# Performance work log

Hardware: AMD Instinct MI355X
Metric: run time of the kernel (lower is better)

The kernel has to match this reference:

```python
import jax, jax.numpy as jnp
import numpy as np

ATTN_HEADS = 4
NEG_INF = float(np.finfo(np.float32).min)


def setup_inputs() -> dict:
    key = jax.random.key(0)
    ks = jax.random.split(key, 7)
    B, N, K, Cin, Cout = 4, 4096, 32, 128, 128
    h_X = jax.random.normal(ks[0], (B, N, Cout), dtype=jnp.float32)
    h_E = jax.random.normal(ks[1], (B, N, K, Cin), dtype=jnp.float32)
    mask_attn = jax.random.randint(ks[2], (B, N, K), 0, 2, dtype=jnp.int32)
    # torch Linear weights are [out_features, in_features]
    W_Q = jax.random.normal(ks[3], (Cout, Cout), dtype=jnp.float32) / np.sqrt(Cout)
    W_K = jax.random.normal(ks[4], (Cout, Cin), dtype=jnp.float32) / np.sqrt(Cin)
    W_V = jax.random.normal(ks[5], (Cout, Cin), dtype=jnp.float32) / np.sqrt(Cin)
    W_O = jax.random.normal(ks[6], (Cout, 3 * Cout), dtype=jnp.float32) / np.sqrt(3 * Cout)
    return {"h_X": h_X, "h_E": h_E, "mask_attn": mask_attn,
            "W_Q": W_Q, "W_K": W_K, "W_V": W_V, "W_O": W_O}


def reference(h_X, h_E, mask_attn, W_Q, W_K, W_V, W_O):
    B, N, K, _ = h_E.shape
    C = W_Q.shape[0]
    H = ATTN_HEADS
    d = C // H

    h_q = (h_X @ W_Q.T).reshape(B, N, H, d)          # [B,N,H,d]
    h_k = (h_E @ W_K.T).reshape(B, N, K, H, d)       # [B,N,K,H,d]
    h_v = (h_E @ W_V.T).reshape(B, N, K, H, d)       # [B,N,K,H,d]

    # per-node, per-head scores over K neighbors
    scores = jnp.einsum('bnhd,bnkhd->bnhk', h_q, h_k) / np.sqrt(d)

    mask = (mask_attn[:, :, None, :] > 0)            # [B,N,1,K] -> broadcast over heads
    logits = jnp.where(mask, scores, NEG_INF)
    attn = jax.nn.softmax(logits, axis=-1) * mask.astype(scores.dtype)  # [B,N,H,K]

    attn_sum = attn.sum(axis=-1, keepdims=True) + 1e-8                  # [B,N,H,1]
    hv_t = jnp.swapaxes(h_v, 2, 3)                                      # [B,N,H,K,d]
    weighted_v = attn[..., None] * hv_t                                 # [B,N,H,K,d]
    weighted_sum = weighted_v.sum(axis=3)                               # [B,N,H,d]
    aggr_mean = (weighted_sum / attn_sum).reshape(B, N, C)
    aggr_sum = weighted_sum.reshape(B, N, C)
    aggr_max = weighted_v.max(axis=3).reshape(B, N, C)

    aggr_cat = jnp.concatenate([aggr_mean, aggr_sum, aggr_max], axis=-1)  # [B,N,3C]
    return aggr_cat @ W_O.T                                               # [B,N,C]
```

## Files before the change

kernel.cpp:

```cpp
#include <hip/hip_runtime.h>
#include <stdint.h>


typedef __attribute__((ext_vector_type(8))) short short8;
typedef __attribute__((ext_vector_type(4))) float f32x4;

#define NPB   16
#define CDIM  128
#define KN    32
#define ESTR  136
#define TSTR  136
#define QSTR  136
#define CATS  392
#define SSTR  36

__device__ __forceinline__ float bf2f(short s) {
    union { unsigned int u; float f; } v;
    v.u = ((unsigned int)(unsigned short)s) << 16;
    return v.f;
}
__device__ __forceinline__ short f2bf(float f) {
    union { float ff; unsigned int u; } v; v.ff = f;
    unsigned int u = v.u;
    u += 0x7FFFu + ((u >> 16) & 1u);
    return (short)(u >> 16);
}

template<bool FP32>
__device__ __forceinline__ short8 load8bf(const void* p, size_t idx) {
    if constexpr (FP32) {
        const float* fp = (const float*)p + idx;
        f32x4 a = *(const f32x4*)fp;
        f32x4 b = *(const f32x4*)(fp + 4);
        short8 r;
        r[0] = f2bf(a[0]); r[1] = f2bf(a[1]); r[2] = f2bf(a[2]); r[3] = f2bf(a[3]);
        r[4] = f2bf(b[0]); r[5] = f2bf(b[1]); r[6] = f2bf(b[2]); r[7] = f2bf(b[3]);
        return r;
    } else {
        return *(const short8*)((const short*)p + idx);
    }
}

template<bool FP32>
__device__ __forceinline__ short loadbf1(const void* p, size_t idx) {
    if constexpr (FP32) return f2bf(((const float*)p)[idx]);
    else return ((const short*)p)[idx];
}

struct alignas(16) Smem {
    short sE[128 * ESTR];
    short sT[64 * TSTR];
    short sQ[16 * QSTR];
    short sCat[16 * CATS];
    float sS[16 * SSTR];
    int   sMask[NPB * KN];
};

template<bool FP32>
__device__ __forceinline__ void issueE(const void* hE, size_t base, int tid,
                                       f32x4 (&eF)[8][2], short8 (&eB)[8]) {
    if constexpr (FP32) {
        #pragma unroll
        for (int it = 0; it < 8; ++it) {
            const float* p = (const float*)hE + base + (size_t)(it * 256 + tid) * 8;
            eF[it][0] = *(const f32x4*)p;
            eF[it][1] = *(const f32x4*)(p + 4);
        }
    } else {
        #pragma unroll
        for (int it = 0; it < 8; ++it)
            eB[it] = *(const short8*)((const short*)hE + base + (size_t)(it * 256 + tid) * 8);
    }
    __builtin_amdgcn_sched_barrier(0);
}

template<bool FP32>
__device__ __forceinline__ void writeE(short* sE, int tid,
                                       const f32x4 (&eF)[8][2], const short8 (&eB)[8]) {
    #pragma unroll
    for (int it = 0; it < 8; ++it) {
        const int chunk = it * 256 + tid, row = chunk >> 4, cc = chunk & 15;
        short8 v;
        if constexpr (FP32) {
            #pragma unroll
            for (int t = 0; t < 4; ++t) { v[t] = f2bf(eF[it][0][t]); v[4 + t] = f2bf(eF[it][1][t]); }
        } else v = eB[it];
        *(short8*)&sE[row * ESTR + cc * 8] = v;
    }
}

template<bool FP32>
__device__ __forceinline__ void na_body(Smem& sm,
    const void* __restrict__ hX, const void* __restrict__ hE,
    const int* __restrict__ mask, const void* __restrict__ WQ,
    const void* __restrict__ WK, const void* __restrict__ WV,
    const void* __restrict__ WO, void* __restrict__ out)
{
    const int tid  = threadIdx.x;
    const int lane = tid & 63;
    const int w    = tid >> 6;
    const int quad = lane >> 4;
    const int l15  = lane & 15;
    const int nb   = blockIdx.x * NPB;
    const size_t ebase = (size_t)nb * (KN * CDIM);

    f32x4 eF[8][2]; short8 eB[8];
    issueE<FP32>(hE, ebase, tid, eF, eB);

    *(int2*)&sm.sMask[tid * 2] = *(const int2*)&mask[(size_t)nb * KN + tid * 2];

    short8 ax[4];
    #pragma unroll
    for (int kk = 0; kk < 4; ++kk)
        ax[kk] = load8bf<FP32>(hX, (size_t)(nb + l15) * CDIM + kk * 32 + quad * 8);

    short8 bq[2][4];
    #pragma unroll
    for (int t2 = 0; t2 < 2; ++t2)
        #pragma unroll
        for (int kk = 0; kk < 4; ++kk)
            bq[t2][kk] = load8bf<FP32>(WQ, (size_t)(w * 32 + t2 * 16 + l15) * CDIM + kk * 32 + quad * 8);

    short8 bk[2][4];
    #pragma unroll
    for (int t2 = 0; t2 < 2; ++t2)
        #pragma unroll
        for (int kk = 0; kk < 4; ++kk) {
            const int j = w * 32 + t2 * 16 + l15;
            short8 b;
            #pragma unroll
            for (int jj = 0; jj < 8; ++jj)
                b[jj] = loadbf1<FP32>(WK, (size_t)(kk * 32 + quad * 8 + jj) * CDIM + j);
            bk[t2][kk] = b;
        }

    {
        f32x4 o0 = {0.f,0.f,0.f,0.f}, o1 = {0.f,0.f,0.f,0.f};
        #pragma unroll
        for (int kk = 0; kk < 4; ++kk) {
            o0 = __builtin_amdgcn_mfma_f32_16x16x32_bf16(ax[kk], bq[0][kk], o0, 0, 0, 0);
            o1 = __builtin_amdgcn_mfma_f32_16x16x32_bf16(ax[kk], bq[1][kk], o1, 0, 0, 0);
        }
        #pragma unroll
        for (int r = 0; r < 4; ++r) {
            const int n = quad * 4 + r;
            sm.sQ[n * QSTR + w * 32 + l15]      = f2bf(o0[r]);
            sm.sQ[n * QSTR + w * 32 + 16 + l15] = f2bf(o1[r]);
        }
    }
    __syncthreads();

    {
        const float scale = 0.17677669529663687f;
        const short8 zz = {0,0,0,0,0,0,0,0};
        #pragma unroll
        for (int m = 0; m < 4; ++m) {
            const int n_g = m * 4 + (l15 >> 2), h_ = l15 & 3;
            const short8 qv = *(const short8*)&sm.sQ[n_g * QSTR + h_ * 32 + quad * 8];
            f32x4 c0 = {0.f,0.f,0.f,0.f}, c1 = {0.f,0.f,0.f,0.f};
            #pragma unroll
            for (int kk = 0; kk < 4; ++kk) {
                const short8 af = (kk == h_) ? qv : zz;
                c0 = __builtin_amdgcn_mfma_f32_16x16x32_bf16(af, bk[0][kk], c0, 0, 0, 0);
                c1 = __builtin_amdgcn_mfma_f32_16x16x32_bf16(af, bk[1][kk], c1, 0, 0, 0);
            }
            #pragma unroll
            for (int r = 0; r < 4; ++r) {
                const int row = m * 16 + quad * 4 + r;
                sm.sT[row * TSTR + w * 32 + l15]      = f2bf(c0[r] * scale);
                sm.sT[row * TSTR + w * 32 + 16 + l15] = f2bf(c1[r] * scale);
            }
        }
    }

    writeE<FP32>(sm.sE, tid, eF, eB);
    issueE<FP32>(hE, ebase + 1 * 128 * 128, tid, eF, eB);
    __syncthreads();

    #pragma unroll 1
    for (int s = 0; s < 4; ++s) {
        short8 bs[4], a0[4], a1[4];
        #pragma unroll
        for (int kk = 0; kk < 4; ++kk) {
            bs[kk] = *(const short8*)&sm.sT[(16 * s + l15) * TSTR + kk * 32 + quad * 8];
            a0[kk] = *(const short8*)&sm.sE[(w * 32 + l15) * ESTR + kk * 32 + quad * 8];
            a1[kk] = *(const short8*)&sm.sE[(w * 32 + 16 + l15) * ESTR + kk * 32 + quad * 8];
        }
        if (s < 3) {
            __syncthreads();
            writeE<FP32>(sm.sE, tid, eF, eB);
            if (s < 2) issueE<FP32>(hE, ebase + (size_t)(s + 2) * 128 * 128, tid, eF, eB);
        }

        f32x4 s0 = {0.f,0.f,0.f,0.f}, s1 = {0.f,0.f,0.f,0.f};
        #pragma unroll
        for (int kk = 0; kk < 4; ++kk) {
            s0 = __builtin_amdgcn_mfma_f32_16x16x32_bf16(a0[kk], bs[kk], s0, 0, 0, 0);
            s1 = __builtin_amdgcn_mfma_f32_16x16x32_bf16(a1[kk], bs[kk], s1, 0, 0, 0);
        }

        {
            const int* mp = &sm.sMask[(s * 4 + (l15 >> 2)) * KN];
            float x[8]; int mk[8];
            #pragma unroll
            for (int j = 0; j < 4; ++j) {
                x[j] = s0[j];     mk[j]     = mp[quad * 4 + j];
                x[4 + j] = s1[j]; mk[4 + j] = mp[16 + quad * 4 + j];
            }
            float m = -3.0e38f;
            #pragma unroll
            for (int j = 0; j < 8; ++j) m = fmaxf(m, (mk[j] > 0) ? x[j] : -3.0e38f);
            m = fmaxf(m, __shfl_xor(m, 16));
            m = fmaxf(m, __shfl_xor(m, 32));
            float dsum = 0.f;
            #pragma unroll
            for (int j = 0; j < 8; ++j) {
                const float e = __expf(fminf(x[j] - m, 0.f)) * ((mk[j] > 0) ? 1.f : 0.f);
                x[j] = e; dsum += e;
            }
            dsum += __shfl_xor(dsum, 16);
            dsum += __shfl_xor(dsum, 32);
            const float inv = (dsum > 0.f) ? (1.f / dsum) : 0.f;
            if ((l15 >> 2) == w) {
                float* sp = &sm.sS[(w * 4 + (l15 & 3)) * SSTR];
                #pragma unroll
                for (int j = 0; j < 4; ++j) {
                    sp[quad * 4 + j]      = x[j] * inv;
                    sp[16 + quad * 4 + j] = x[4 + j] * inv;
                }
                if (quad == 0)
                    sp[33] = 1.0f / (((dsum > 0.f) ? 1.0f : 0.0f) + 1e-8f);
            }
        }

        #pragma unroll
        for (int ct = 0; ct < 8; ++ct) {
            const int h = ct >> 1;
            f32x4 av0 = {0.f,0.f,0.f,0.f}, av1 = {0.f,0.f,0.f,0.f};
            #pragma unroll
            for (int kk = 0; kk < 4; ++kk) {
                const short8 bvf = load8bf<FP32>(WV, (size_t)(ct * 16 + l15) * CDIM + kk * 32 + quad * 8);
                av0 = __builtin_amdgcn_mfma_f32_16x16x32_bf16(a0[kk], bvf, av0, 0, 0, 0);
                av1 = __builtin_amdgcn_mfma_f32_16x16x32_bf16(a1[kk], bvf, av1, 0, 0, 0);
            }
            const float* ap = &sm.sS[(w * 4 + h) * SSTR];
            const float ainv = ap[33];
            float sum = 0.f, mx = -3.0e38f;
            #pragma unroll
            for (int r = 0; r < 4; ++r) {
                const float p0 = ap[quad * 4 + r]      * av0[r];
                const float p1 = ap[16 + quad * 4 + r] * av1[r];
                sum += p0 + p1;
                mx = fmaxf(mx, fmaxf(p0, p1));
            }
            sum += __shfl_xor(sum, 16);
            sum += __shfl_xor(sum, 32);
            mx = fmaxf(mx, __shfl_xor(mx, 16));
            mx = fmaxf(mx, __shfl_xor(mx, 32));
            if (quad == 0) {
                const int c = ct * 16 + l15, row = s * 4 + w;
                sm.sCat[row * CATS + c]       = f2bf(sum * ainv);
                sm.sCat[row * CATS + 128 + c] = f2bf(sum);
                sm.sCat[row * CATS + 256 + c] = f2bf(mx);
            }
        }

        if (s < 3) __syncthreads();
    }
    __syncthreads();

    {
        f32x4 o0 = {0.f,0.f,0.f,0.f}, o1 = {0.f,0.f,0.f,0.f};
        #pragma unroll
        for (int kk = 0; kk < 12; ++kk) {
            const short8 a  = *(const short8*)&sm.sCat[l15 * CATS + kk * 32 + quad * 8];
            const short8 b0 = load8bf<FP32>(WO, (size_t)(w * 32 + l15) * 384 + kk * 32 + quad * 8);
            const short8 b1 = load8bf<FP32>(WO, (size_t)(w * 32 + 16 + l15) * 384 + kk * 32 + quad * 8);
            o0 = __builtin_amdgcn_mfma_f32_16x16x32_bf16(a, b0, o0, 0, 0, 0);
            o1 = __builtin_amdgcn_mfma_f32_16x16x32_bf16(a, b1, o1, 0, 0, 0);
        }
        #pragma unroll
        for (int r = 0; r < 4; ++r) {
            const int node = quad * 4 + r;
            const size_t base = (size_t)(nb + node) * CDIM + w * 32;
            if constexpr (FP32) {
                ((float*)out)[base + l15]      = o0[r];
                ((float*)out)[base + 16 + l15] = o1[r];
            } else {
                ((short*)out)[base + l15]      = f2bf(o0[r]);
                ((short*)out)[base + 16 + l15] = f2bf(o1[r]);
            }
        }
    }
}

__global__ __launch_bounds__(256, 2)
void na_fused(const void* __restrict__ hX, const void* __restrict__ hE,
              const int* __restrict__ mask, const void* __restrict__ WQ,
              const void* __restrict__ WK, const void* __restrict__ WV,
              const void* __restrict__ WO, void* __restrict__ out)
{
    __shared__ Smem sm;
    const short* wq16 = (const short*)WQ;
    const int lane = threadIdx.x & 63;
    int cnt = 0;
    #pragma unroll
    for (int i = 0; i < 8; ++i) {
        const float v = bf2f(wq16[lane + i * 64]);
        if (!(fabsf(v) < 8.0f)) cnt++;
    }
    #pragma unroll
    for (int d = 1; d < 64; d <<= 1) cnt += __shfl_xor(cnt, d);
    if (cnt > 16) na_body<true >(sm, hX, hE, mask, WQ, WK, WV, WO, out);
    else          na_body<false>(sm, hX, hE, mask, WQ, WK, WV, WO, out);
}

extern "C" void kernel_launch(void* const* d_in, const int* in_sizes, int n_in,
                              void* d_out, int out_size, void* d_ws, size_t ws_size,
                              hipStream_t stream) {
    (void)in_sizes; (void)n_in; (void)ws_size; (void)out_size; (void)d_ws;
    const void* hX   = d_in[0];
    const void* hE   = d_in[1];
    const int*  mask = (const int*)d_in[2];
    const void* WQ   = d_in[3];
    const void* WK   = d_in[4];
    const void* WV   = d_in[5];
    const void* WO   = d_in[6];

    na_fused<<<dim3(1024), dim3(256), 0, stream>>>(hX, hE, mask, WQ, WK, WV, WO, d_out);
}
```

Before: 431.0 us.

## Split fused kernel into Q/T, attention, and output projection kernels

Splits the single fused kernel into three launches. The first computes Q and the per-head transformed keys T into workspace. The second streams h_E with T double-buffered, keeps WV fragments in registers, and reorganizes the value loop per node so WV is no longer reloaded from global memory inside the inner loop; it writes the concatenated aggregates to workspace. The third performs the output projection. This lowers register and LDS pressure per kernel for higher occupancy, at the cost of extra global round-trips through workspace and additional launch overhead.

```diff
diff --git a/kernel.cpp b/kernel.cpp
--- a/kernel.cpp
+++ b/kernel.cpp
@@ -5,13 +5,9 @@
 typedef __attribute__((ext_vector_type(8))) short short8;
 typedef __attribute__((ext_vector_type(4))) float f32x4;
 
-#define NPB   16
 #define CDIM  128
 #define KN    32
 #define ESTR  136
-#define TSTR  136
-#define QSTR  136
-#define CATS  392
 #define SSTR  36
 
 __device__ __forceinline__ float bf2f(short s) {
@@ -47,11 +43,117 @@
     else return ((const short*)p)[idx];
 }
 
-struct alignas(16) Smem {
+__device__ __forceinline__ bool detect_fp32(const short* wp) {
+    const int lane = threadIdx.x & 63;
+    int cnt = 0;
+    #pragma unroll
+    for (int i = 0; i < 8; ++i) {
+        const float v = bf2f(wp[lane + i * 64]);
+        if (!(fabsf(v) < 8.0f)) cnt++;
+    }
+    #pragma unroll
+    for (int d = 1; d < 64; d <<= 1) cnt += __shfl_xor(cnt, d);
+    return cnt > 16;
+}
+
+#define ANPB 64
+struct alignas(16) SmemA {
+    short sX[ANPB * ESTR];
+    short sQ[ANPB * ESTR];
+};
+
+template<bool FP32>
+__device__ __forceinline__ void naA_body(SmemA& sm, const void* __restrict__ hX,
+    const void* __restrict__ WQ, const void* __restrict__ WK, short* __restrict__ Tg)
+{
+    const int tid = threadIdx.x, lane = tid & 63, w = tid >> 6;
+    const int quad = lane >> 4, l15 = lane & 15;
+    const int nbA = blockIdx.x * ANPB;
+
+    #pragma unroll
+    for (int it = 0; it < 4; ++it) {
+        const int chunk = it * 256 + tid, row = chunk >> 4, cc = chunk & 15;
+        *(short8*)&sm.sX[row * ESTR + cc * 8] =
+            load8bf<FP32>(hX, (size_t)nbA * CDIM + (size_t)chunk * 8);
+    }
+    short8 bq[2][4];
+    #pragma unroll
+    for (int t2 = 0; t2 < 2; ++t2)
+        #pragma unroll
+        for (int kk = 0; kk < 4; ++kk)
+            bq[t2][kk] = load8bf<FP32>(WQ, (size_t)(w * 32 + t2 * 16 + l15) * CDIM + kk * 32 + quad * 8);
+    __syncthreads();
+
+    #pragma unroll
+    for (int mt = 0; mt < 4; ++mt) {
+        short8 ax[4];
+        #pragma unroll
+        for (int kk = 0; kk < 4; ++kk)
+            ax[kk] = *(const short8*)&sm.sX[(mt * 16 + l15) * ESTR + kk * 32 + quad * 8];
+        f32x4 o0 = {0.f,0.f,0.f,0.f}, o1 = {0.f,0.f,0.f,0.f};
+        #pragma unroll
+        for (int kk = 0; kk < 4; ++kk) {
+            o0 = __builtin_amdgcn_mfma_f32_16x16x32_bf16(ax[kk], bq[0][kk], o0, 0, 0, 0);
+            o1 = __builtin_amdgcn_mfma_f32_16x16x32_bf16(ax[kk], bq[1][kk], o1, 0, 0, 0);
+        }
+        #pragma unroll
+        for (int r = 0; r < 4; ++r) {
+            const int row = mt * 16 + quad * 4 + r;
+            sm.sQ[row * ESTR + w * 32 + l15]      = f2bf(o0[r]);
+            sm.sQ[row * ESTR + w * 32 + 16 + l15] = f2bf(o1[r]);
+        }
+    }
+    __syncthreads();
+
+    short8 bk[2][4];
+    #pragma unroll
+    for (int t2 = 0; t2 < 2; ++t2)
+        #pragma unroll
+        for (int kk = 0; kk < 4; ++kk) {
+            const int j = w * 32 + t2 * 16 + l15;
+            short8 b;
+            #pragma unroll
+            for (int jj = 0; jj < 8; ++jj)
+                b[jj] = loadbf1<FP32>(WK, (size_t)(kk * 32 + quad * 8 + jj) * CDIM + j);
+            bk[t2][kk] = b;
+        }
+
+    const float scale = 0.17677669529663687f;
+    const short8 zz = {0,0,0,0,0,0,0,0};
+    #pragma unroll
+    for (int m = 0; m < 16; ++m) {
+        const int n_g = (m * 16 + l15) >> 2, h_ = l15 & 3;
+        const short8 qv = *(const short8*)&sm.sQ[n_g * ESTR + h_ * 32 + quad * 8];
+        f32x4 c0 = {0.f,0.f,0.f,0.f}, c1 = {0.f,0.f,0.f,0.f};
+        #pragma unroll
+        for (int kk = 0; kk < 4; ++kk) {
+            const short8 af = (kk == h_) ? qv : zz;
+            c0 = __builtin_amdgcn_mfma_f32_16x16x32_bf16(af, bk[0][kk], c0, 0, 0, 0);
+            c1 = __builtin_amdgcn_mfma_f32_16x16x32_bf16(af, bk[1][kk], c1, 0, 0, 0);
+        }
+        #pragma unroll
+        for (int r = 0; r < 4; ++r) {
+            const int rg = m * 16 + quad * 4 + r;
+            const size_t base = (size_t)(nbA + (rg >> 2)) * 512 + (rg & 3) * 128 + w * 32;
+            Tg[base + l15]      = f2bf(c0[r] * scale);
+            Tg[base + 16 + l15] = f2bf(c1[r] * scale);
+        }
+    }
+}
+
+__global__ __launch_bounds__(256, 3)
+void naA(const void* __restrict__ hX, const void* __restrict__ WQ,
+         const void* __restrict__ WK, short* __restrict__ Tg)
+{
+    __shared__ SmemA sm;
+    if (detect_fp32((const short*)WQ)) naA_body<true >(sm, hX, WQ, WK, Tg);
+    else                               naA_body<false>(sm, hX, WQ, WK, Tg);
+}
+
+#define NPB 16
+struct alignas(16) SmemB {
     short sE[128 * ESTR];
-    short sT[64 * TSTR];
-    short sQ[16 * QSTR];
-    short sCat[16 * CATS];
+    short sTb[2][16 * ESTR];
     float sS[16 * SSTR];
     int   sMask[NPB * KN];
 };
@@ -71,7 +173,6 @@
         for (int it = 0; it < 8; ++it)
             eB[it] = *(const short8*)((const short*)hE + base + (size_t)(it * 256 + tid) * 8);
     }
-    __builtin_amdgcn_sched_barrier(0);
 }
 
 template<bool FP32>
@@ -90,108 +191,48 @@
 }
 
 template<bool FP32>
-__device__ __forceinline__ void na_body(Smem& sm,
-    const void* __restrict__ hX, const void* __restrict__ hE,
-    const int* __restrict__ mask, const void* __restrict__ WQ,
-    const void* __restrict__ WK, const void* __restrict__ WV,
-    const void* __restrict__ WO, void* __restrict__ out)
-{
-    const int tid  = threadIdx.x;
-    const int lane = tid & 63;
-    const int w    = tid >> 6;
-    const int quad = lane >> 4;
-    const int l15  = lane & 15;
-    const int nb   = blockIdx.x * NPB;
+__device__ __forceinline__ void naB_body(SmemB& sm, const void* __restrict__ hE,
+    const int* __restrict__ mask, const void* __restrict__ WV,
+    const short* __restrict__ Tg, short* __restrict__ catG)
+{
+    const int tid = threadIdx.x, lane = tid & 63, w = tid >> 6;
+    const int quad = lane >> 4, l15 = lane & 15;
+    const int nb = blockIdx.x * NPB;
     const size_t ebase = (size_t)nb * (KN * CDIM);
 
-    f32x4 eF[8][2]; short8 eB[8];
+    f32x4 eF[8][2]; short8 eB[8]; short8 eT;
     issueE<FP32>(hE, ebase, tid, eF, eB);
+    eT = *(const short8*)(Tg + (size_t)nb * 512 + tid * 8);
+    __builtin_amdgcn_sched_barrier(0);
 
     *(int2*)&sm.sMask[tid * 2] = *(const int2*)&mask[(size_t)nb * KN + tid * 2];
 
-    short8 ax[4];
-    #pragma unroll
-    for (int kk = 0; kk < 4; ++kk)
-        ax[kk] = load8bf<FP32>(hX, (size_t)(nb + l15) * CDIM + kk * 32 + quad * 8);
-
-    short8 bq[2][4];
-    #pragma unroll
-    for (int t2 = 0; t2 < 2; ++t2)
+    short8 bv[2][4];
+    #pragma unroll
+    for (int ct2 = 0; ct2 < 2; ++ct2)
         #pragma unroll
         for (int kk = 0; kk < 4; ++kk)
-            bq[t2][kk] = load8bf<FP32>(WQ, (size_t)(w * 32 + t2 * 16 + l15) * CDIM + kk * 32 + quad * 8);
-
-    short8 bk[2][4];
-    #pragma unroll
-    for (int t2 = 0; t2 < 2; ++t2)
-        #pragma unroll
-        for (int kk = 0; kk < 4; ++kk) {
-            const int j = w * 32 + t2 * 16 + l15;
-            short8 b;
-            #pragma unroll
-            for (int jj = 0; jj < 8; ++jj)
-                b[jj] = loadbf1<FP32>(WK, (size_t)(kk * 32 + quad * 8 + jj) * CDIM + j);
-            bk[t2][kk] = b;
-        }
-
-    {
-        f32x4 o0 = {0.f,0.f,0.f,0.f}, o1 = {0.f,0.f,0.f,0.f};
-        #pragma unroll
-        for (int kk = 0; kk < 4; ++kk) {
-            o0 = __builtin_amdgcn_mfma_f32_16x16x32_bf16(ax[kk], bq[0][kk], o0, 0, 0, 0);
-            o1 = __builtin_amdgcn_mfma_f32_16x16x32_bf16(ax[kk], bq[1][kk], o1, 0, 0, 0);
-        }
-        #pragma unroll
-        for (int r = 0; r < 4; ++r) {
-            const int n = quad * 4 + r;
-            sm.sQ[n * QSTR + w * 32 + l15]      = f2bf(o0[r]);
-            sm.sQ[n * QSTR + w * 32 + 16 + l15] = f2bf(o1[r]);
-        }
-    }
-    __syncthreads();
-
-    {
-        const float scale = 0.17677669529663687f;
-        const short8 zz = {0,0,0,0,0,0,0,0};
-        #pragma unroll
-        for (int m = 0; m < 4; ++m) {
-            const int n_g = m * 4 + (l15 >> 2), h_ = l15 & 3;
-            const short8 qv = *(const short8*)&sm.sQ[n_g * QSTR + h_ * 32 + quad * 8];
-            f32x4 c0 = {0.f,0.f,0.f,0.f}, c1 = {0.f,0.f,0.f,0.f};
-            #pragma unroll
-            for (int kk = 0; kk < 4; ++kk) {
-                const short8 af = (kk == h_) ? qv : zz;
-                c0 = __builtin_amdgcn_mfma_f32_16x16x32_bf16(af, bk[0][kk], c0, 0, 0, 0);
-                c1 = __builtin_amdgcn_mfma_f32_16x16x32_bf16(af, bk[1][kk], c1, 0, 0, 0);
-            }
-            #pragma unroll
-            for (int r = 0; r < 4; ++r) {
-                const int row = m * 16 + quad * 4 + r;
-                sm.sT[row * TSTR + w * 32 + l15]      = f2bf(c0[r] * scale);
-                sm.sT[row * TSTR + w * 32 + 16 + l15] = f2bf(c1[r] * scale);
-            }
-        }
-    }
+            bv[ct2][kk] = load8bf<FP32>(WV, (size_t)((2 * w + ct2) * 16 + l15) * CDIM + kk * 32 + quad * 8);
 
     writeE<FP32>(sm.sE, tid, eF, eB);
-    issueE<FP32>(hE, ebase + 1 * 128 * 128, tid, eF, eB);
+    { const int row = tid >> 4, cc = tid & 15;
+      *(short8*)&sm.sTb[0][row * ESTR + cc * 8] = eT; }
+    issueE<FP32>(hE, ebase + 128 * 128, tid, eF, eB);
+    eT = *(const short8*)(Tg + (size_t)(nb + 4) * 512 + tid * 8);
+    __builtin_amdgcn_sched_barrier(0);
     __syncthreads();
 
     #pragma unroll 1
     for (int s = 0; s < 4; ++s) {
+        const short* tb = sm.sTb[s & 1];
+
         short8 bs[4], a0[4], a1[4];
         #pragma unroll
         for (int kk = 0; kk < 4; ++kk) {
-            bs[kk] = *(const short8*)&sm.sT[(16 * s + l15) * TSTR + kk * 32 + quad * 8];
+            bs[kk] = *(const short8*)&tb[l15 * ESTR + kk * 32 + quad * 8];
             a0[kk] = *(const short8*)&sm.sE[(w * 32 + l15) * ESTR + kk * 32 + quad * 8];
             a1[kk] = *(const short8*)&sm.sE[(w * 32 + 16 + l15) * ESTR + kk * 32 + quad * 8];
         }
-        if (s < 3) {
-            __syncthreads();
-            writeE<FP32>(sm.sE, tid, eF, eB);
-            if (s < 2) issueE<FP32>(hE, ebase + (size_t)(s + 2) * 128 * 128, tid, eF, eB);
-        }
-
         f32x4 s0 = {0.f,0.f,0.f,0.f}, s1 = {0.f,0.f,0.f,0.f};
         #pragma unroll
         for (int kk = 0; kk < 4; ++kk) {
@@ -232,93 +273,130 @@
                     sp[33] = 1.0f / (((dsum > 0.f) ? 1.0f : 0.0f) + 1e-8f);
             }
         }
-
-        #pragma unroll
-        for (int ct = 0; ct < 8; ++ct) {
-            const int h = ct >> 1;
-            f32x4 av0 = {0.f,0.f,0.f,0.f}, av1 = {0.f,0.f,0.f,0.f};
+        __syncthreads();
+
+        #pragma unroll
+        for (int n_ = 0; n_ < 4; ++n_) {
+            short8 c0[4], c1[4];
             #pragma unroll
             for (int kk = 0; kk < 4; ++kk) {
-                const short8 bvf = load8bf<FP32>(WV, (size_t)(ct * 16 + l15) * CDIM + kk * 32 + quad * 8);
-                av0 = __builtin_amdgcn_mfma_f32_16x16x32_bf16(a0[kk], bvf, av0, 0, 0, 0);
-                av1 = __builtin_amdgcn_mfma_f32_16x16x32_bf16(a1[kk], bvf, av1, 0, 0, 0);
-            }
-            const float* ap = &sm.sS[(w * 4 + h) * SSTR];
+                c0[kk] = *(const short8*)&sm.sE[(n_ * 32 + l15) * ESTR + kk * 32 + quad * 8];
+                c1[kk] = *(const short8*)&sm.sE[(n_ * 32 + 16 + l15) * ESTR + kk * 32 + quad * 8];
+            }
+            const float* ap = &sm.sS[(n_ * 4 + w) * SSTR];
             const float ainv = ap[33];
-            float sum = 0.f, mx = -3.0e38f;
-            #pragma unroll
-            for (int r = 0; r < 4; ++r) {
-                const float p0 = ap[quad * 4 + r]      * av0[r];
-                const float p1 = ap[16 + quad * 4 + r] * av1[r];
-                sum += p0 + p1;
-                mx = fmaxf(mx, fmaxf(p0, p1));
-            }
-            sum += __shfl_xor(sum, 16);
-            sum += __shfl_xor(sum, 32);
-            mx = fmaxf(mx, __shfl_xor(mx, 16));
-            mx = fmaxf(mx, __shfl_xor(mx, 32));
-            if (quad == 0) {
-                const int c = ct * 16 + l15, row = s * 4 + w;
-                sm.sCat[row * CATS + c]       = f2bf(sum * ainv);
-                sm.sCat[row * CATS + 128 + c] = f2bf(sum);
-                sm.sCat[row * CATS + 256 + c] = f2bf(mx);
-            }
-        }
-
-        if (s < 3) __syncthreads();
+            #pragma unroll
+            for (int ct2 = 0; ct2 < 2; ++ct2) {
+                f32x4 av0 = {0.f,0.f,0.f,0.f}, av1 = {0.f,0.f,0.f,0.f};
+                #pragma unroll
+                for (int kk = 0; kk < 4; ++kk) {
+                    av0 = __builtin_amdgcn_mfma_f32_16x16x32_bf16(c0[kk], bv[ct2][kk], av0, 0, 0, 0);
+                    av1 = __builtin_amdgcn_mfma_f32_16x16x32_bf16(c1[kk], bv[ct2][kk], av1, 0, 0, 0);
+                }
+                float sum = 0.f, mx = -3.0e38f;
+                #pragma unroll
+                for (int r = 0; r < 4; ++r) {
+                    const float p0 = ap[quad * 4 + r]      * av0[r];
+                    const float p1 = ap[16 + quad * 4 + r] * av1[r];
+                    sum += p0 + p1;
+                    mx = fmaxf(mx, fmaxf(p0, p1));
+                }
+                sum += __shfl_xor(sum, 16);
+                sum += __shfl_xor(sum, 32);
+                mx = fmaxf(mx, __shfl_xor(mx, 16));
+                mx = fmaxf(mx, __shfl_xor(mx, 32));
+                if (quad == 0) {
+                    const int c = (2 * w + ct2) * 16 + l15;
+                    const size_t ng = (size_t)(nb + s * 4 + n_) * 384;
+                    catG[ng + c]       = f2bf(sum * ainv);
+                    catG[ng + 128 + c] = f2bf(sum);
+                    catG[ng + 256 + c] = f2bf(mx);
+                }
+            }
+        }
+        __syncthreads();
+
+        if (s < 3) {
+            writeE<FP32>(sm.sE, tid, eF, eB);
+            { const int row = tid >> 4, cc = tid & 15;
+              *(short8*)&sm.sTb[(s + 1) & 1][row * ESTR + cc * 8] = eT; }
+            if (s < 2) {
+                issueE<FP32>(hE, ebase + (size_t)(s + 2) * 128 * 128, tid, eF, eB);
+                eT = *(const short8*)(Tg + (size_t)(nb + (s + 2) * 4) * 512 + tid * 8);
+                __builtin_amdgcn_sched_barrier(0);
+            }
+            __syncthreads();
+        }
+    }
+}
+
+__global__ __launch_bounds__(256, 3)
+void naB(const void* __restrict__ hE, const int* __restrict__ mask,
+         const void* __restrict__ WV, const short* __restrict__ Tg,
+         short* __restrict__ catG)
+{
+    __shared__ SmemB sm;
+    if (detect_fp32((const short*)WV)) naB_body<true >(sm, hE, mask, WV, Tg, catG);
+    else                               naB_body<false>(sm, hE, mask, WV, Tg, catG);
+}
+
+struct alignas(16) SmemC {
+    short sCat[16 * 392];
+};
+
+template<bool FP32>
+__device__ __forceinline__ void naC_body(SmemC& sm, const short* __restrict__ catG,
+    const void* __restrict__ WO, void* __restrict__ out)
+{
+    const int tid = threadIdx.x, lane = tid & 63, w = tid >> 6;
+    const int quad = lane >> 4, l15 = lane & 15;
+    const int nb = blockIdx.x * 16;
+
+    #pragma unroll
+    for (int it = 0; it < 3; ++it) {
+        const int chunk = it * 256 + tid;
+        const int row = chunk / 48, cc = chunk % 48;
+        *(short8*)&sm.sCat[row * 392 + cc * 8] =
+            *(const short8*)&catG[(size_t)nb * 384 + (size_t)chunk * 8];
     }
     __syncthreads();
 
-    {
-        f32x4 o0 = {0.f,0.f,0.f,0.f}, o1 = {0.f,0.f,0.f,0.f};
-        #pragma unroll
-        for (int kk = 0; kk < 12; ++kk) {
-            const short8 a  = *(const short8*)&sm.sCat[l15 * CATS + kk * 32 + quad * 8];
-            const short8 b0 = load8bf<FP32>(WO, (size_t)(w * 32 + l15) * 384 + kk * 32 + quad * 8);
-            const short8 b1 = load8bf<FP32>(WO, (size_t)(w * 32 + 16 + l15) * 384 + kk * 32 + quad * 8);
-            o0 = __builtin_amdgcn_mfma_f32_16x16x32_bf16(a, b0, o0, 0, 0, 0);
-            o1 = __builtin_amdgcn_mfma_f32_16x16x32_bf16(a, b1, o1, 0, 0, 0);
-        }
-        #pragma unroll
-        for (int r = 0; r < 4; ++r) {
-            const int node = quad * 4 + r;
-            const size_t base = (size_t)(nb + node) * CDIM + w * 32;
-            if constexpr (FP32) {
-                ((float*)out)[base + l15]      = o0[r];
-                ((float*)out)[base + 16 + l15] = o1[r];
-            } else {
-                ((short*)out)[base + l15]      = f2bf(o0[r]);
-                ((short*)out)[base + 16 + l15] = f2bf(o1[r]);
-            }
-        }
-    }
-}
-
-__global__ __launch_bounds__(256, 2)
-void na_fused(const void* __restrict__ hX, const void* __restrict__ hE,
-              const int* __restrict__ mask, const void* __restrict__ WQ,
-              const void* __restrict__ WK, const void* __restrict__ WV,
-              const void* __restrict__ WO, void* __restrict__ out)
-{
-    __shared__ Smem sm;
-    const short* wq16 = (const short*)WQ;
-    const int lane = threadIdx.x & 63;
-    int cnt = 0;
-    #pragma unroll
-    for (int i = 0; i < 8; ++i) {
-        const float v = bf2f(wq16[lane + i * 64]);
-        if (!(fabsf(v) < 8.0f)) cnt++;
-    }
-    #pragma unroll
-    for (int d = 1; d < 64; d <<= 1) cnt += __shfl_xor(cnt, d);
-    if (cnt > 16) na_body<true >(sm, hX, hE, mask, WQ, WK, WV, WO, out);
-    else          na_body<false>(sm, hX, hE, mask, WQ, WK, WV, WO, out);
+    f32x4 o0 = {0.f,0.f,0.f,0.f}, o1 = {0.f,0.f,0.f,0.f};
+    #pragma unroll
+    for (int kk = 0; kk < 12; ++kk) {
+        const short8 a  = *(const short8*)&sm.sCat[l15 * 392 + kk * 32 + quad * 8];
+        const short8 b0 = load8bf<FP32>(WO, (size_t)(w * 32 + l15) * 384 + kk * 32 + quad * 8);
+        const short8 b1 = load8bf<FP32>(WO, (size_t)(w * 32 + 16 + l15) * 384 + kk * 32 + quad * 8);
+        o0 = __builtin_amdgcn_mfma_f32_16x16x32_bf16(a, b0, o0, 0, 0, 0);
+        o1 = __builtin_amdgcn_mfma_f32_16x16x32_bf16(a, b1, o1, 0, 0, 0);
+    }
+    #pragma unroll
+    for (int r = 0; r < 4; ++r) {
+        const int node = quad * 4 + r;
+        const size_t base = (size_t)(nb + node) * CDIM + w * 32;
+        if constexpr (FP32) {
+            ((float*)out)[base + l15]      = o0[r];
+            ((float*)out)[base + 16 + l15] = o1[r];
+        } else {
+            ((short*)out)[base + l15]      = f2bf(o0[r]);
+            ((short*)out)[base + 16 + l15] = f2bf(o1[r]);
+        }
+    }
+}
+
+__global__ __launch_bounds__(256, 4)
+void naC(const short* __restrict__ catG, const void* __restrict__ WO,
+         void* __restrict__ out)
+{
+    __shared__ SmemC sm;
+    if (detect_fp32((const short*)WO)) naC_body<true >(sm, catG, WO, out);
+    else                               naC_body<false>(sm, catG, WO, out);
 }
 
 extern "C" void kernel_launch(void* const* d_in, const int* in_sizes, int n_in,
                               void* d_out, int out_size, void* d_ws, size_t ws_size,
                               hipStream_t stream) {
-    (void)in_sizes; (void)n_in; (void)ws_size; (void)out_size; (void)d_ws;
+    (void)in_sizes; (void)n_in; (void)ws_size; (void)out_size;
     const void* hX   = d_in[0];
     const void* hE   = d_in[1];
     const int*  mask = (const int*)d_in[2];
@@ -327,5 +405,10 @@
     const void* WV   = d_in[5];
     const void* WO   = d_in[6];
 
-    na_fused<<<dim3(1024), dim3(256), 0, stream>>>(hX, hE, mask, WQ, WK, WV, WO, d_out);
-}
+    short* Tg   = (short*)d_ws;
+    short* catG = (short*)((char*)d_ws + (32u << 20));
+
+    naA<<<dim3(256),  dim3(256), 0, stream>>>(hX, WQ, WK, Tg);
+    naB<<<dim3(1024), dim3(256), 0, stream>>>(hE, mask, WV, Tg, catG);
+    naC<<<dim3(1024), dim3(256), 0, stream>>>(catG, WO, d_out);
+}
```

Result: no change. 434.0 us (+0.7%).

## Hoist W_V fragments into registers and reassign value-projection work per wave

Applied to the files above, without the earlier changes.

Each wave now keeps its slice of W_V output columns in registers for the whole kernel. It computes value projections for all nodes in the stage by reading the E tile from shared memory, instead of reloading and converting W_V from global memory for every output tile in every stage. The E-tile refill for the next stage moves to after aggregation, which adds an extra barrier per stage and reduces how much the global-load latency is hidden. fp32-to-bf16 conversion switches to the packed __float22bfloat162_rn intrinsic, and register pressure rises from the resident W_V fragments.

```diff
diff --git a/kernel.cpp b/kernel.cpp
--- a/kernel.cpp
+++ b/kernel.cpp
@@ -1,4 +1,5 @@
 #include <hip/hip_runtime.h>
+#include <hip/hip_bf16.h>
 #include <stdint.h>
 
 
@@ -9,10 +10,9 @@
 #define CDIM  128
 #define KN    32
 #define ESTR  136
-#define TSTR  136
-#define QSTR  136
 #define CATS  392
 #define SSTR  36
+#define NEGI  -3.0e38f
 
 __device__ __forceinline__ float bf2f(short s) {
     union { unsigned int u; float f; } v;
@@ -26,16 +26,27 @@
     return (short)(u >> 16);
 }
 
+__device__ __forceinline__ short8 cvt8(const f32x4& a, const f32x4& b) {
+    union { __hip_bfloat162 h; unsigned int u; } c0, c1, c2, c3;
+    c0.h = __float22bfloat162_rn(float2{a[0], a[1]});
+    c1.h = __float22bfloat162_rn(float2{a[2], a[3]});
+    c2.h = __float22bfloat162_rn(float2{b[0], b[1]});
+    c3.h = __float22bfloat162_rn(float2{b[2], b[3]});
+    short8 r;
+    r[0] = (short)(c0.u & 0xffff); r[1] = (short)(c0.u >> 16);
+    r[2] = (short)(c1.u & 0xffff); r[3] = (short)(c1.u >> 16);
+    r[4] = (short)(c2.u & 0xffff); r[5] = (short)(c2.u >> 16);
+    r[6] = (short)(c3.u & 0xffff); r[7] = (short)(c3.u >> 16);
+    return r;
+}
+
 template<bool FP32>
 __device__ __forceinline__ short8 load8bf(const void* p, size_t idx) {
     if constexpr (FP32) {
         const float* fp = (const float*)p + idx;
         f32x4 a = *(const f32x4*)fp;
         f32x4 b = *(const f32x4*)(fp + 4);
-        short8 r;
-        r[0] = f2bf(a[0]); r[1] = f2bf(a[1]); r[2] = f2bf(a[2]); r[3] = f2bf(a[3]);
-        r[4] = f2bf(b[0]); r[5] = f2bf(b[1]); r[6] = f2bf(b[2]); r[7] = f2bf(b[3]);
-        return r;
+        return cvt8(a, b);
     } else {
         return *(const short8*)((const short*)p + idx);
     }
@@ -47,10 +58,23 @@
     else return ((const short*)p)[idx];
 }
 
+__device__ __forceinline__ bool detect_fp32(const short* wp) {
+    const int lane = threadIdx.x & 63;
+    int cnt = 0;
+    #pragma unroll
+    for (int i = 0; i < 8; ++i) {
+        const float v = bf2f(wp[lane + i * 64]);
+        if (!(fabsf(v) < 8.0f)) cnt++;
+    }
+    #pragma unroll
+    for (int d = 1; d < 64; d <<= 1) cnt += __shfl_xor(cnt, d);
+    return cnt > 16;
+}
+
 struct alignas(16) Smem {
     short sE[128 * ESTR];
-    short sT[64 * TSTR];
-    short sQ[16 * QSTR];
+    short sT[64 * ESTR];
+    short sQ[16 * ESTR];
     short sCat[16 * CATS];
     float sS[16 * SSTR];
     int   sMask[NPB * KN];
@@ -81,10 +105,8 @@
     for (int it = 0; it < 8; ++it) {
         const int chunk = it * 256 + tid, row = chunk >> 4, cc = chunk & 15;
         short8 v;
-        if constexpr (FP32) {
-            #pragma unroll
-            for (int t = 0; t < 4; ++t) { v[t] = f2bf(eF[it][0][t]); v[4 + t] = f2bf(eF[it][1][t]); }
-        } else v = eB[it];
+        if constexpr (FP32) v = cvt8(eF[it][0], eF[it][1]);
+        else                v = eB[it];
         *(short8*)&sE[row * ESTR + cc * 8] = v;
     }
 }
@@ -113,13 +135,28 @@
     #pragma unroll
     for (int kk = 0; kk < 4; ++kk)
         ax[kk] = load8bf<FP32>(hX, (size_t)(nb + l15) * CDIM + kk * 32 + quad * 8);
-
     short8 bq[2][4];
     #pragma unroll
     for (int t2 = 0; t2 < 2; ++t2)
         #pragma unroll
         for (int kk = 0; kk < 4; ++kk)
             bq[t2][kk] = load8bf<FP32>(WQ, (size_t)(w * 32 + t2 * 16 + l15) * CDIM + kk * 32 + quad * 8);
+
+    {
+        f32x4 o0 = {0.f,0.f,0.f,0.f}, o1 = {0.f,0.f,0.f,0.f};
+        #pragma unroll
+        for (int kk = 0; kk < 4; ++kk) {
+            o0 = __builtin_amdgcn_mfma_f32_16x16x32_bf16(ax[kk], bq[0][kk], o0, 0, 0, 0);
+            o1 = __builtin_amdgcn_mfma_f32_16x16x32_bf16(ax[kk], bq[1][kk], o1, 0, 0, 0);
+        }
+        #pragma unroll
+        for (int r = 0; r < 4; ++r) {
+            const int n = quad * 4 + r;
+            sm.sQ[n * ESTR + w * 32 + l15]      = f2bf(o0[r]);
+            sm.sQ[n * ESTR + w * 32 + 16 + l15] = f2bf(o1[r]);
+        }
+    }
+    __syncthreads();
 
     short8 bk[2][4];
     #pragma unroll
@@ -135,28 +172,12 @@
         }
 
     {
-        f32x4 o0 = {0.f,0.f,0.f,0.f}, o1 = {0.f,0.f,0.f,0.f};
-        #pragma unroll
-        for (int kk = 0; kk < 4; ++kk) {
-            o0 = __builtin_amdgcn_mfma_f32_16x16x32_bf16(ax[kk], bq[0][kk], o0, 0, 0, 0);
-            o1 = __builtin_amdgcn_mfma_f32_16x16x32_bf16(ax[kk], bq[1][kk], o1, 0, 0, 0);
-        }
-        #pragma unroll
-        for (int r = 0; r < 4; ++r) {
-            const int n = quad * 4 + r;
-            sm.sQ[n * QSTR + w * 32 + l15]      = f2bf(o0[r]);
-            sm.sQ[n * QSTR + w * 32 + 16 + l15] = f2bf(o1[r]);
-        }
-    }
-    __syncthreads();
-
-    {
         const float scale = 0.17677669529663687f;
         const short8 zz = {0,0,0,0,0,0,0,0};
         #pragma unroll
         for (int m = 0; m < 4; ++m) {
             const int n_g = m * 4 + (l15 >> 2), h_ = l15 & 3;
-            const short8 qv = *(const short8*)&sm.sQ[n_g * QSTR + h_ * 32 + quad * 8];
+            const short8 qv = *(const short8*)&sm.sQ[n_g * ESTR + h_ * 32 + quad * 8];
             f32x4 c0 = {0.f,0.f,0.f,0.f}, c1 = {0.f,0.f,0.f,0.f};
             #pragma unroll
             for (int kk = 0; kk < 4; ++kk) {
@@ -167,11 +188,18 @@
             #pragma unroll
             for (int r = 0; r < 4; ++r) {
                 const int row = m * 16 + quad * 4 + r;
-                sm.sT[row * TSTR + w * 32 + l15]      = f2bf(c0[r] * scale);
-                sm.sT[row * TSTR + w * 32 + 16 + l15] = f2bf(c1[r] * scale);
-            }
-        }
-    }
+                sm.sT[row * ESTR + w * 32 + l15]      = f2bf(c0[r] * scale);
+                sm.sT[row * ESTR + w * 32 + 16 + l15] = f2bf(c1[r] * scale);
+            }
+        }
+    }
+
+    short8 bv[2][4];
+    #pragma unroll
+    for (int ct2 = 0; ct2 < 2; ++ct2)
+        #pragma unroll
+        for (int kk = 0; kk < 4; ++kk)
+            bv[ct2][kk] = load8bf<FP32>(WV, (size_t)((2 * w + ct2) * 16 + l15) * CDIM + kk * 32 + quad * 8);
 
     writeE<FP32>(sm.sE, tid, eF, eB);
     issueE<FP32>(hE, ebase + 1 * 128 * 128, tid, eF, eB);
@@ -182,16 +210,10 @@
         short8 bs[4], a0[4], a1[4];
         #pragma unroll
         for (int kk = 0; kk < 4; ++kk) {
-            bs[kk] = *(const short8*)&sm.sT[(16 * s + l15) * TSTR + kk * 32 + quad * 8];
+            bs[kk] = *(const short8*)&sm.sT[(16 * s + l15) * ESTR + kk * 32 + quad * 8];
             a0[kk] = *(const short8*)&sm.sE[(w * 32 + l15) * ESTR + kk * 32 + quad * 8];
             a1[kk] = *(const short8*)&sm.sE[(w * 32 + 16 + l15) * ESTR + kk * 32 + quad * 8];
         }
-        if (s < 3) {
-            __syncthreads();
-            writeE<FP32>(sm.sE, tid, eF, eB);
-            if (s < 2) issueE<FP32>(hE, ebase + (size_t)(s + 2) * 128 * 128, tid, eF, eB);
-        }
-
         f32x4 s0 = {0.f,0.f,0.f,0.f}, s1 = {0.f,0.f,0.f,0.f};
         #pragma unroll
         for (int kk = 0; kk < 4; ++kk) {
@@ -207,9 +229,9 @@
                 x[j] = s0[j];     mk[j]     = mp[quad * 4 + j];
                 x[4 + j] = s1[j]; mk[4 + j] = mp[16 + quad * 4 + j];
             }
-            float m = -3.0e38f;
-            #pragma unroll
-            for (int j = 0; j < 8; ++j) m = fmaxf(m, (mk[j] > 0) ? x[j] : -3.0e38f);
+            float m = NEGI;
+            #pragma unroll
+            for (int j = 0; j < 8; ++j) m = fmaxf(m, (mk[j] > 0) ? x[j] : NEGI);
             m = fmaxf(m, __shfl_xor(m, 16));
             m = fmaxf(m, __shfl_xor(m, 32));
             float dsum = 0.f;
@@ -232,42 +254,54 @@
                     sp[33] = 1.0f / (((dsum > 0.f) ? 1.0f : 0.0f) + 1e-8f);
             }
         }
-
-        #pragma unroll
-        for (int ct = 0; ct < 8; ++ct) {
-            const int h = ct >> 1;
-            f32x4 av0 = {0.f,0.f,0.f,0.f}, av1 = {0.f,0.f,0.f,0.f};
+        __syncthreads();
+
+        #pragma unroll
+        for (int n_ = 0; n_ < 4; ++n_) {
+            short8 c0[4], c1[4];
             #pragma unroll
             for (int kk = 0; kk < 4; ++kk) {
-                const short8 bvf = load8bf<FP32>(WV, (size_t)(ct * 16 + l15) * CDIM + kk * 32 + quad * 8);
-                av0 = __builtin_amdgcn_mfma_f32_16x16x32_bf16(a0[kk], bvf, av0, 0, 0, 0);
-                av1 = __builtin_amdgcn_mfma_f32_16x16x32_bf16(a1[kk], bvf, av1, 0, 0, 0);
-            }
-            const float* ap = &sm.sS[(w * 4 + h) * SSTR];
+                c0[kk] = *(const short8*)&sm.sE[(n_ * 32 + l15) * ESTR + kk * 32 + quad * 8];
+                c1[kk] = *(const short8*)&sm.sE[(n_ * 32 + 16 + l15) * ESTR + kk * 32 + quad * 8];
+            }
+            const float* ap = &sm.sS[(n_ * 4 + w) * SSTR];
             const float ainv = ap[33];
-            float sum = 0.f, mx = -3.0e38f;
-            #pragma unroll
-            for (int r = 0; r < 4; ++r) {
-                const float p0 = ap[quad * 4 + r]      * av0[r];
-                const float p1 = ap[16 + quad * 4 + r] * av1[r];
-                sum += p0 + p1;
-                mx = fmaxf(mx, fmaxf(p0, p1));
-            }
-            sum += __shfl_xor(sum, 16);
-            sum += __shfl_xor(sum, 32);
-            mx = fmaxf(mx, __shfl_xor(mx, 16));
-            mx = fmaxf(mx, __shfl_xor(mx, 32));
-            if (quad == 0) {
-                const int c = ct * 16 + l15, row = s * 4 + w;
-                sm.sCat[row * CATS + c]       = f2bf(sum * ainv);
-                sm.sCat[row * CATS + 128 + c] = f2bf(sum);
-                sm.sCat[row * CATS + 256 + c] = f2bf(mx);
-            }
-        }
-
-        if (s < 3) __syncthreads();
-    }
-    __syncthreads();
+            #pragma unroll
+            for (int ct2 = 0; ct2 < 2; ++ct2) {
+                f32x4 av0 = {0.f,0.f,0.f,0.f}, av1 = {0.f,0.f,0.f,0.f};
+                #pragma unroll
+                for (int kk = 0; kk < 4; ++kk) {
+                    av0 = __builtin_amdgcn_mfma_f32_16x16x32_bf16(c0[kk], bv[ct2][kk], av0, 0, 0, 0);
+                    av1 = __builtin_amdgcn_mfma_f32_16x16x32_bf16(c1[kk], bv[ct2][kk], av1, 0, 0, 0);
+                }
+                float sum = 0.f, mx = NEGI;
+                #pragma unroll
+                for (int r = 0; r < 4; ++r) {
+                    const float p0 = ap[quad * 4 + r]      * av0[r];
+                    const float p1 = ap[16 + quad * 4 + r] * av1[r];
+                    sum += p0 + p1;
+                    mx = fmaxf(mx, fmaxf(p0, p1));
+                }
+                sum += __shfl_xor(sum, 16);
+                sum += __shfl_xor(sum, 32);
+                mx = fmaxf(mx, __shfl_xor(mx, 16));
+                mx = fmaxf(mx, __shfl_xor(mx, 32));
+                if (quad == 0) {
+                    const int c = (2 * w + ct2) * 16 + l15, row = s * 4 + n_;
+                    sm.sCat[row * CATS + c]       = f2bf(sum * ainv);
+                    sm.sCat[row * CATS + 128 + c] = f2bf(sum);
+                    sm.sCat[row * CATS + 256 + c] = f2bf(mx);
+                }
+            }
+        }
+        __syncthreads();
+
+        if (s < 3) {
+            writeE<FP32>(sm.sE, tid, eF, eB);
+            if (s < 2) issueE<FP32>(hE, ebase + (size_t)(s + 2) * 128 * 128, tid, eF, eB);
+            __syncthreads();
+        }
+    }
 
     {
         f32x4 o0 = {0.f,0.f,0.f,0.f}, o1 = {0.f,0.f,0.f,0.f};
@@ -301,18 +335,8 @@
               const void* __restrict__ WO, void* __restrict__ out)
 {
     __shared__ Smem sm;
-    const short* wq16 = (const short*)WQ;
-    const int lane = threadIdx.x & 63;
-    int cnt = 0;
-    #pragma unroll
-    for (int i = 0; i < 8; ++i) {
-        const float v = bf2f(wq16[lane + i * 64]);
-        if (!(fabsf(v) < 8.0f)) cnt++;
-    }
-    #pragma unroll
-    for (int d = 1; d < 64; d <<= 1) cnt += __shfl_xor(cnt, d);
-    if (cnt > 16) na_body<true >(sm, hX, hE, mask, WQ, WK, WV, WO, out);
-    else          na_body<false>(sm, hX, hE, mask, WQ, WK, WV, WO, out);
+    if (detect_fp32((const short*)WQ)) na_body<true >(sm, hX, hE, mask, WQ, WK, WV, WO, out);
+    else                               na_body<false>(sm, hX, hE, mask, WQ, WK, WV, WO, out);
 }
 
 extern "C" void kernel_launch(void* const* d_in, const int* in_sizes, int n_in,
```

Result: faster. 401.2 us (-6.9%).
